# Optimization experiments

Measured on AMD Instinct MI355X. Metric: run time of the kernel, lower is better.

## Reference

```python
import jax, jax.numpy as jnp
import numpy as np

HIDDEN = 128
NUM_BLOCKS = 8
BLOCK = HIDDEN // NUM_BLOCKS  # 16
HSF = 1                       # hidden_size_factor
LAMBDA = 0.01                 # sparsity_threshold (softshrink)
SCALE = 0.02


def softshrink(v, lam):
    return jnp.sign(v) * jnp.maximum(jnp.abs(v) - lam, 0.0)


def setup_inputs() -> dict:
    key = jax.random.key(0)
    k0, k1, k2, k3, k4 = jax.random.split(key, 5)
    x = jax.random.normal(k0, (4, HIDDEN, 256, 256), dtype=jnp.float32)
    w1 = SCALE * jax.random.normal(k1, (2, NUM_BLOCKS, BLOCK, BLOCK * HSF), dtype=jnp.float32)
    b1 = SCALE * jax.random.normal(k2, (2, NUM_BLOCKS, BLOCK * HSF), dtype=jnp.float32)
    w2 = SCALE * jax.random.normal(k3, (2, NUM_BLOCKS, BLOCK * HSF, BLOCK), dtype=jnp.float32)
    b2 = SCALE * jax.random.normal(k4, (2, NUM_BLOCKS, BLOCK), dtype=jnp.float32)
    return {"x": x, "w1": w1, "b1": b1, "w2": w2, "b2": b2}


def reference(x, w1, b1, w2, b2):
    bias = x
    B, C, H, W = x.shape
    xf = jnp.fft.rfft2(x.astype(jnp.float32), axes=(2, 3), norm='ortho')  # [B,C,H,Wf] complex
    Wf = xf.shape[3]
    xb = xf.reshape(B, NUM_BLOCKS, BLOCK, H, Wf)
    xr, xi = xb.real, xb.imag

    mm = lambda a, w: jnp.einsum('bkihw,kio->bkohw', a, w)
    o1r = jax.nn.relu(mm(xr, w1[0]) - mm(xi, w1[1]) + b1[0][None, :, :, None, None])
    o1i = jax.nn.relu(mm(xi, w1[0]) + mm(xr, w1[1]) + b1[1][None, :, :, None, None])
    o2r = mm(o1r, w2[0]) - mm(o1i, w2[1]) + b2[0][None, :, :, None, None]
    o2i = mm(o1i, w2[0]) + mm(o1r, w2[1]) + b2[1][None, :, :, None, None]

    sr = softshrink(o2r, LAMBDA)
    si = softshrink(o2i, LAMBDA)
    xc = (sr + 1j * si).reshape(B, C, H, Wf) * xf
    out = jnp.fft.irfft2(xc, s=(H, W), axes=(2, 3), norm='ortho').astype(x.dtype)
    return out + bias
```

## Files before the change

### kernel.cpp

```cpp
#include <hip/hip_runtime.h>
#include <math.h>

#define Bn 4
#define Cn 128
#define Hn 256
#define Wn 256
#define WFn 129
#define NBn 8
#define BLn 16
#define LAMv 0.01f
#define LSTR 272

#define C1c 0.9238795325112867f
#define S1c 0.3826834323650898f
#define RTc 0.7071067811865476f

__device__ constexpr int rev4(int j) {
  return ((j & 1) << 3) | ((j & 2) << 1) | ((j & 4) >> 1) | ((j & 8) >> 3);
}

__device__ __forceinline__ float2 pkfma(float2 a, float2 b, float2 c) {
  return make_float2(fmaf(a.x, b.x, c.x), fmaf(a.y, b.y, c.y));
}

__device__ __forceinline__ void init_twt(float2* twt, int t) {
  int s = t >> 4, k2 = t & 15;
  float sn, cs;
  sincospif((float)(s * k2) / 128.0f, &sn, &cs);
  twt[t] = make_float2(cs, -sn);
}

template <int SIGN>
__device__ __forceinline__ void fft16(float* xr, float* xi) {
  const float g = (SIGN > 0) ? 1.0f : -1.0f;
  {
    const float WC[8] = {1.f, C1c, RTc, S1c, 0.f, -S1c, -RTc, -C1c};
    const float WS[8] = {0.f, -S1c, -RTc, -C1c, -1.f, -C1c, -RTc, -S1c};
#pragma unroll
    for (int j = 0; j < 8; j++) {
      float ur = xr[j], ui = xi[j], vr = xr[j + 8], vi = xi[j + 8];
      float dr = ur - vr, di = ui - vi;
      xr[j] = ur + vr; xi[j] = ui + vi;
      float wc = WC[j], ws = g * WS[j];
      xr[j + 8] = dr * wc - di * ws;
      xi[j + 8] = dr * ws + di * wc;
    }
  }
  {
    const float WC[4] = {1.f, RTc, 0.f, -RTc};
    const float WS[4] = {0.f, -RTc, -1.f, -RTc};
#pragma unroll
    for (int b = 0; b < 16; b += 8)
#pragma unroll
      for (int j = 0; j < 4; j++) {
        float ur = xr[b + j], ui = xi[b + j];
        float vr = xr[b + j + 4], vi = xi[b + j + 4];
        float dr = ur - vr, di = ui - vi;
        xr[b + j] = ur + vr; xi[b + j] = ui + vi;
        float wc = WC[j], ws = g * WS[j];
        xr[b + j + 4] = dr * wc - di * ws;
        xi[b + j + 4] = dr * ws + di * wc;
      }
  }
  {
#pragma unroll
    for (int b = 0; b < 16; b += 4) {
      {
        float ur = xr[b], ui = xi[b], vr = xr[b + 2], vi = xi[b + 2];
        xr[b] = ur + vr; xi[b] = ui + vi;
        xr[b + 2] = ur - vr; xi[b + 2] = ui - vi;
      }
      {
        float ur = xr[b + 1], ui = xi[b + 1], vr = xr[b + 3], vi = xi[b + 3];
        float dr = ur - vr, di = ui - vi;
        xr[b + 1] = ur + vr; xi[b + 1] = ui + vi;
        xr[b + 3] = g * di;
        xi[b + 3] = -g * dr;
      }
    }
  }
  {
#pragma unroll
    for (int b = 0; b < 16; b += 2) {
      float ur = xr[b], ui = xi[b], vr = xr[b + 1], vi = xi[b + 1];
      xr[b] = ur + vr; xi[b] = ui + vi;
      xr[b + 1] = ur - vr; xi[b + 1] = ui - vi;
    }
  }
}

template <int SIGN>
__device__ __forceinline__ void fft256_4step(float* vr, float* vi,
                                             float* re, float* im, int s,
                                             const float2* twt) {
  fft16<SIGN>(vr, vi);
#pragma unroll
  for (int j = 1; j < 16; j++) {
    const int k2 = rev4(j);
    float2 w = twt[s * 16 + k2];
    float wc = w.x;
    float ws = (SIGN > 0) ? w.y : -w.y;
    float r = vr[j] * wc - vi[j] * ws;
    vi[j] = vr[j] * ws + vi[j] * wc;
    vr[j] = r;
  }
  __syncthreads();
#pragma unroll
  for (int j = 0; j < 16; j++) {
    const int k2 = rev4(j);
    const int p = k2 * 16 + (s ^ k2);
    re[p] = vr[j]; im[p] = vi[j];
  }
  __syncthreads();
#pragma unroll
  for (int n1 = 0; n1 < 16; n1++) {
    const int p = s * 16 + (n1 ^ s);
    vr[n1] = re[p]; vi[n1] = im[p];
  }
  __syncthreads();
  fft16<SIGN>(vr, vi);
}

__global__ __launch_bounds__(256) void k_rowfft(const float* __restrict__ x,
                                                float2* __restrict__ S) {
  int blk = blockIdx.x;
  int bc = blk >> 3;
  int h0 = (blk & 7) << 5;
  __shared__ __align__(16) float zr[16][LSTR], zi[16][LSTR];
  __shared__ __align__(16) float2 twt[256];
  int t = threadIdx.x;
  init_twt(&twt[0], t);
  const float4* xrow =
      (const float4*)(x + (size_t)bc * (Hn * Wn) + (size_t)h0 * Wn);
  const float sc = 1.0f / 256.0f;
#pragma unroll
  for (int j = 0; j < 8; j++) {
    int f4 = t + j * 256;
    float4 v = xrow[f4];
    int r = f4 >> 6;
    int i = (f4 << 2) & 255;
    float* dst = (r & 1) ? &zi[r >> 1][i] : &zr[r >> 1][i];
    *(float4*)dst = make_float4(v.x * sc, v.y * sc, v.z * sc, v.w * sc);
  }
  __syncthreads();
  int p = t >> 4, s = t & 15;
  float vr[16], vi[16];
#pragma unroll
  for (int m = 0; m < 16; m++) {
    vr[m] = zr[p][s + 16 * m];
    vi[m] = zi[p][s + 16 * m];
  }
  fft256_4step<1>(vr, vi, &zr[p][0], &zi[p][0], s, &twt[0]);
#pragma unroll
  for (int j = 0; j < 16; j++) {
    int h = 16 * rev4(j) + s;
    zr[p][h] = vr[j]; zi[p][h] = vi[j];
  }
  __syncthreads();
  for (int f = t; f < WFn * 32; f += 256) {
    int wf = f >> 5, rr = f & 31;
    int pp = rr >> 1;
    int nk = (256 - wf) & 255;
    float zkr = zr[pp][wf], zki = zi[pp][wf];
    float znr = zr[pp][nk], zni = zi[pp][nk];
    float re_, im_;
    if ((rr & 1) == 0) { re_ = 0.5f * (zkr + znr); im_ = 0.5f * (zki - zni); }
    else               { re_ = 0.5f * (zki + zni); im_ = 0.5f * (znr - zkr); }
    S[((size_t)bc * WFn + wf) * Hn + (h0 + rr)] = make_float2(re_, im_);
  }
}

__global__ __launch_bounds__(256) void k_spectral(float2* __restrict__ S,
                                                  const float* __restrict__ w1,
                                                  const float* __restrict__ b1,
                                                  const float* __restrict__ w2,
                                                  const float* __restrict__ b2) {
  int blk = blockIdx.x;
  int wcol = blk % WFn;
  int bk = blk / WFn;
  int k = bk & 7;
  int b = bk >> 3;
  __shared__ __align__(16) float ar[16][LSTR], ai[16][LSTR];
  __shared__ __align__(16) float2 twt[256];
  __shared__ __align__(16) float w1r[256], w1i[256], w2r[256], w2i[256];
  __shared__ float b1r[16], b1i[16], b2r[16], b2i[16];
  int t = threadIdx.x;
  init_twt(&twt[0], t);
  w1r[t] = w1[k * 256 + t];        w1i[t] = w1[(8 + k) * 256 + t];
  w2r[t] = w2[k * 256 + t];        w2i[t] = w2[(8 + k) * 256 + t];
  if (t < 16) {
    b1r[t] = b1[k * 16 + t];       b1i[t] = b1[(8 + k) * 16 + t];
    b2r[t] = b2[k * 16 + t];       b2i[t] = b2[(8 + k) * 16 + t];
  }
  __syncthreads();
  int c = t >> 4, s = t & 15;
  float2* col = S + ((size_t)(b * Cn + k * BLn + c) * WFn + wcol) * Hn;
  float vr[16], vi[16];
#pragma unroll
  for (int m = 0; m < 16; m++) {
    float2 z = col[s + 16 * m];
    vr[m] = z.x; vi[m] = z.y;
  }
  fft256_4step<1>(vr, vi, &ar[c][0], &ai[c][0], s, &twt[0]);
#pragma unroll
  for (int j = 0; j < 16; j++) {
    int h = 16 * rev4(j) + s;
    ar[c][h] = vr[j]; ai[c][h] = vi[j];
  }
  __syncthreads();

  {
    const int h = t;
    const float4* W1R = (const float4*)w1r;
    const float4* W1I = (const float4*)w1i;
    const float4* W2R = (const float4*)w2r;
    const float4* W2I = (const float4*)w2i;
    float2 o1p[8], o1q[8];
#pragma unroll
    for (int q = 0; q < 8; q++) {
      o1p[q] = make_float2(b1r[2 * q], b1r[2 * q + 1]);
      o1q[q] = make_float2(b1i[2 * q], b1i[2 * q + 1]);
    }
#pragma unroll
    for (int i = 0; i < 16; i++) {
      float xr_ = ar[i][h], xi_ = ai[i][h];
      float2 xr2 = make_float2(xr_, xr_);
      float2 xi2 = make_float2(xi_, xi_);
      float2 xn2 = make_float2(-xi_, -xi_);
#pragma unroll
      for (int oq = 0; oq < 4; oq++) {
        float4 wr = W1R[i * 4 + oq];
        float4 wi = W1I[i * 4 + oq];
        float2 wr0 = make_float2(wr.x, wr.y), wr1 = make_float2(wr.z, wr.w);
        float2 wi0 = make_float2(wi.x, wi.y), wi1 = make_float2(wi.z, wi.w);
        o1p[2 * oq + 0] = pkfma(xr2, wr0, pkfma(xn2, wi0, o1p[2 * oq + 0]));
        o1p[2 * oq + 1] = pkfma(xr2, wr1, pkfma(xn2, wi1, o1p[2 * oq + 1]));
        o1q[2 * oq + 0] = pkfma(xi2, wr0, pkfma(xr2, wi0, o1q[2 * oq + 0]));
        o1q[2 * oq + 1] = pkfma(xi2, wr1, pkfma(xr2, wi1, o1q[2 * oq + 1]));
      }
    }
#pragma unroll
    for (int q = 0; q < 8; q++) {
      o1p[q] = make_float2(fmaxf(o1p[q].x, 0.f), fmaxf(o1p[q].y, 0.f));
      o1q[q] = make_float2(fmaxf(o1q[q].x, 0.f), fmaxf(o1q[q].y, 0.f));
    }
    float2 o2p[8], o2q[8];
#pragma unroll
    for (int q = 0; q < 8; q++) {
      o2p[q] = make_float2(b2r[2 * q], b2r[2 * q + 1]);
      o2q[q] = make_float2(b2i[2 * q], b2i[2 * q + 1]);
    }
#pragma unroll
    for (int i = 0; i < 16; i++) {
      float pr = (i & 1) ? o1p[i >> 1].y : o1p[i >> 1].x;
      float pi_ = (i & 1) ? o1q[i >> 1].y : o1q[i >> 1].x;
      float2 pr2 = make_float2(pr, pr);
      float2 pi2 = make_float2(pi_, pi_);
      float2 pn2 = make_float2(-pi_, -pi_);
#pragma unroll
      for (int oq = 0; oq < 4; oq++) {
        float4 wr = W2R[i * 4 + oq];
        float4 wi = W2I[i * 4 + oq];
        float2 wr0 = make_float2(wr.x, wr.y), wr1 = make_float2(wr.z, wr.w);
        float2 wi0 = make_float2(wi.x, wi.y), wi1 = make_float2(wi.z, wi.w);
        o2p[2 * oq + 0] = pkfma(pr2, wr0, pkfma(pn2, wi0, o2p[2 * oq + 0]));
        o2p[2 * oq + 1] = pkfma(pr2, wr1, pkfma(pn2, wi1, o2p[2 * oq + 1]));
        o2q[2 * oq + 0] = pkfma(pi2, wr0, pkfma(pr2, wi0, o2q[2 * oq + 0]));
        o2q[2 * oq + 1] = pkfma(pi2, wr1, pkfma(pr2, wi1, o2q[2 * oq + 1]));
      }
    }
#pragma unroll
    for (int o = 0; o < 16; o++) {
      float vr_ = (o & 1) ? o2p[o >> 1].y : o2p[o >> 1].x;
      float vi_ = (o & 1) ? o2q[o >> 1].y : o2q[o >> 1].x;
      float sr = copysignf(fmaxf(fabsf(vr_) - LAMv, 0.0f), vr_);
      float si = copysignf(fmaxf(fabsf(vi_) - LAMv, 0.0f), vi_);
      float fr = ar[o][h], fi = ai[o][h];
      ar[o][h] = sr * fr - si * fi;
      ai[o][h] = sr * fi + si * fr;
    }
  }
  __syncthreads();
#pragma unroll
  for (int m = 0; m < 16; m++) {
    vr[m] = ar[c][s + 16 * m];
    vi[m] = ai[c][s + 16 * m];
  }
  fft256_4step<-1>(vr, vi, &ar[c][0], &ai[c][0], s, &twt[0]);
#pragma unroll
  for (int j = 0; j < 16; j++) {
    int h = 16 * rev4(j) + s;
    col[h] = make_float2(vr[j], vi[j]);
  }
}

__global__ __launch_bounds__(256) void k_invrow(const float2* __restrict__ S,
                                                const float* __restrict__ x,
                                                float* __restrict__ out) {
  int blk = blockIdx.x;
  int bc = blk >> 3;
  int h0 = (blk & 7) << 5;
  __shared__ __align__(16) float zr[16][LSTR], zi[16][LSTR];
  __shared__ __align__(16) float2 twt[256];
  int t = threadIdx.x;
  init_twt(&twt[0], t);
  const float4* S4 = (const float4*)S;
  for (int f = t; f < WFn * 16; f += 256) {
    int wf = f >> 4, p = f & 15;
    float4 v = S4[((size_t)bc * WFn + wf) * (Hn / 2) + (h0 >> 1) + p];
    zr[p][wf] = v.x - v.w;
    zi[p][wf] = v.y + v.z;
    if (wf >= 1 && wf <= 127) {
      zr[p][256 - wf] = v.x + v.w;
      zi[p][256 - wf] = v.z - v.y;
    }
  }
  __syncthreads();
  int p = t >> 4, s = t & 15;
  float vr[16], vi[16];
#pragma unroll
  for (int m = 0; m < 16; m++) {
    vr[m] = zr[p][s + 16 * m];
    vi[m] = zi[p][s + 16 * m];
  }
  fft256_4step<-1>(vr, vi, &zr[p][0], &zi[p][0], s, &twt[0]);
#pragma unroll
  for (int j = 0; j < 16; j++) {
    int w = 16 * rev4(j) + s;
    zr[p][w] = vr[j]; zi[p][w] = vi[j];
  }
  __syncthreads();
  const float sc = 1.0f / 256.0f;
  size_t base = (size_t)bc * (Hn * Wn) + (size_t)h0 * Wn;
  const float4* x4 = (const float4*)(x + base);
  float4* o4 = (float4*)(out + base);
#pragma unroll
  for (int j = 0; j < 8; j++) {
    int f4 = t + j * 256;
    int rr = f4 >> 6;
    int i = (f4 << 2) & 255;
    const float* src = (rr & 1) ? &zi[rr >> 1][i] : &zr[rr >> 1][i];
    float4 v = *(const float4*)src;
    float4 xv = x4[f4];
    o4[f4] = make_float4(fmaf(v.x, sc, xv.x), fmaf(v.y, sc, xv.y),
                         fmaf(v.z, sc, xv.z), fmaf(v.w, sc, xv.w));
  }
}

extern "C" void kernel_launch(void* const* d_in, const int* in_sizes, int n_in,
                              void* d_out, int out_size, void* d_ws,
                              size_t ws_size, hipStream_t stream) {
  const float* x  = (const float*)d_in[0];
  const float* w1 = (const float*)d_in[1];
  const float* b1 = (const float*)d_in[2];
  const float* w2 = (const float*)d_in[3];
  const float* b2 = (const float*)d_in[4];
  float* out = (float*)d_out;
  float2* S = (float2*)d_ws;

  k_rowfft<<<Bn * Cn * (Hn / 32), 256, 0, stream>>>(x, S);
  k_spectral<<<Bn * NBn * WFn, 256, 0, stream>>>(S, w1, b1, w2, b2);
  k_invrow<<<Bn * Cn * (Hn / 32), 256, 0, stream>>>(S, x, out);
}
```

Measured before the change: 458.5 us.

## Process two frequency columns per block in spectral kernel

Each spectral block now handles two adjacent Wf columns, so the twiddle table, weight and bias loads into shared memory are paid once per two columns. The grid shrinks to 65 column pairs per (b,k), and the MLP loop interleaves two independent accumulator sets to give more ILP. The twiddle table is also transposed so that lanes with consecutive s read consecutive entries, which should cut LDS bank conflicts. In exchange, shared memory per block roughly doubles and register pressure rises, which may lower occupancy, and the odd last column runs redundant FFT work on leftover data.

```diff
diff --git a/kernel.cpp b/kernel.cpp
--- a/kernel.cpp
+++ b/kernel.cpp
@@ -24,7 +24,7 @@
 }
 
 __device__ __forceinline__ void init_twt(float2* twt, int t) {
-  int s = t >> 4, k2 = t & 15;
+  int k2 = t >> 4, s = t & 15;
   float sn, cs;
   sincospif((float)(s * k2) / 128.0f, &sn, &cs);
   twt[t] = make_float2(cs, -sn);
@@ -97,7 +97,7 @@
 #pragma unroll
   for (int j = 1; j < 16; j++) {
     const int k2 = rev4(j);
-    float2 w = twt[s * 16 + k2];
+    float2 w = twt[k2 * 16 + s];
     float wc = w.x;
     float ws = (SIGN > 0) ? w.y : -w.y;
     float r = vr[j] * wc - vi[j] * ws;
@@ -176,11 +176,13 @@
                                                   const float* __restrict__ w2,
                                                   const float* __restrict__ b2) {
   int blk = blockIdx.x;
-  int wcol = blk % WFn;
-  int bk = blk / WFn;
+  int wi = blk % 65;
+  int bk = blk / 65;
   int k = bk & 7;
   int b = bk >> 3;
-  __shared__ __align__(16) float ar[16][LSTR], ai[16][LSTR];
+  int wcol0 = wi * 2;
+  const bool has1 = (wcol0 + 1) < WFn;
+  __shared__ __align__(16) float ar[2][16][LSTR], ai[2][16][LSTR];
   __shared__ __align__(16) float2 twt[256];
   __shared__ __align__(16) float w1r[256], w1i[256], w2r[256], w2i[256];
   __shared__ float b1r[16], b1i[16], b2r[16], b2i[16];
@@ -194,18 +196,32 @@
   }
   __syncthreads();
   int c = t >> 4, s = t & 15;
-  float2* col = S + ((size_t)(b * Cn + k * BLn + c) * WFn + wcol) * Hn;
+  float2* col0 = S + ((size_t)(b * Cn + k * BLn + c) * WFn + wcol0) * Hn;
+  float2* col1 = col0 + Hn;
   float vr[16], vi[16];
 #pragma unroll
   for (int m = 0; m < 16; m++) {
-    float2 z = col[s + 16 * m];
+    float2 z = col0[s + 16 * m];
     vr[m] = z.x; vi[m] = z.y;
   }
-  fft256_4step<1>(vr, vi, &ar[c][0], &ai[c][0], s, &twt[0]);
+  fft256_4step<1>(vr, vi, &ar[0][c][0], &ai[0][c][0], s, &twt[0]);
 #pragma unroll
   for (int j = 0; j < 16; j++) {
     int h = 16 * rev4(j) + s;
-    ar[c][h] = vr[j]; ai[c][h] = vi[j];
+    ar[0][c][h] = vr[j]; ai[0][c][h] = vi[j];
+  }
+  if (has1) {
+#pragma unroll
+    for (int m = 0; m < 16; m++) {
+      float2 z = col1[s + 16 * m];
+      vr[m] = z.x; vi[m] = z.y;
+    }
+  }
+  fft256_4step<1>(vr, vi, &ar[1][c][0], &ai[1][c][0], s, &twt[0]);
+#pragma unroll
+  for (int j = 0; j < 16; j++) {
+    int h = 16 * rev4(j) + s;
+    ar[1][c][h] = vr[j]; ai[1][c][h] = vi[j];
   }
   __syncthreads();
 
@@ -215,82 +231,116 @@
     const float4* W1I = (const float4*)w1i;
     const float4* W2R = (const float4*)w2r;
     const float4* W2I = (const float4*)w2i;
-    float2 o1p[8], o1q[8];
+    float2 o1p[2][8], o1q[2][8];
 #pragma unroll
     for (int q = 0; q < 8; q++) {
-      o1p[q] = make_float2(b1r[2 * q], b1r[2 * q + 1]);
-      o1q[q] = make_float2(b1i[2 * q], b1i[2 * q + 1]);
+      float2 bp = make_float2(b1r[2 * q], b1r[2 * q + 1]);
+      float2 bq = make_float2(b1i[2 * q], b1i[2 * q + 1]);
+      o1p[0][q] = bp; o1p[1][q] = bp;
+      o1q[0][q] = bq; o1q[1][q] = bq;
     }
 #pragma unroll
     for (int i = 0; i < 16; i++) {
-      float xr_ = ar[i][h], xi_ = ai[i][h];
-      float2 xr2 = make_float2(xr_, xr_);
-      float2 xi2 = make_float2(xi_, xi_);
-      float2 xn2 = make_float2(-xi_, -xi_);
+      float xr0 = ar[0][i][h], xi0 = ai[0][i][h];
+      float xr1 = ar[1][i][h], xi1 = ai[1][i][h];
+      float2 xr20 = make_float2(xr0, xr0), xi20 = make_float2(xi0, xi0);
+      float2 xn20 = make_float2(-xi0, -xi0);
+      float2 xr21 = make_float2(xr1, xr1), xi21 = make_float2(xi1, xi1);
+      float2 xn21 = make_float2(-xi1, -xi1);
 #pragma unroll
       for (int oq = 0; oq < 4; oq++) {
         float4 wr = W1R[i * 4 + oq];
         float4 wi = W1I[i * 4 + oq];
         float2 wr0 = make_float2(wr.x, wr.y), wr1 = make_float2(wr.z, wr.w);
         float2 wi0 = make_float2(wi.x, wi.y), wi1 = make_float2(wi.z, wi.w);
-        o1p[2 * oq + 0] = pkfma(xr2, wr0, pkfma(xn2, wi0, o1p[2 * oq + 0]));
-        o1p[2 * oq + 1] = pkfma(xr2, wr1, pkfma(xn2, wi1, o1p[2 * oq + 1]));
-        o1q[2 * oq + 0] = pkfma(xi2, wr0, pkfma(xr2, wi0, o1q[2 * oq + 0]));
-        o1q[2 * oq + 1] = pkfma(xi2, wr1, pkfma(xr2, wi1, o1q[2 * oq + 1]));
-      }
-    }
+        o1p[0][2*oq+0] = pkfma(xr20, wr0, pkfma(xn20, wi0, o1p[0][2*oq+0]));
+        o1p[0][2*oq+1] = pkfma(xr20, wr1, pkfma(xn20, wi1, o1p[0][2*oq+1]));
+        o1q[0][2*oq+0] = pkfma(xi20, wr0, pkfma(xr20, wi0, o1q[0][2*oq+0]));
+        o1q[0][2*oq+1] = pkfma(xi20, wr1, pkfma(xr20, wi1, o1q[0][2*oq+1]));
+        o1p[1][2*oq+0] = pkfma(xr21, wr0, pkfma(xn21, wi0, o1p[1][2*oq+0]));
+        o1p[1][2*oq+1] = pkfma(xr21, wr1, pkfma(xn21, wi1, o1p[1][2*oq+1]));
+        o1q[1][2*oq+0] = pkfma(xi21, wr0, pkfma(xr21, wi0, o1q[1][2*oq+0]));
+        o1q[1][2*oq+1] = pkfma(xi21, wr1, pkfma(xr21, wi1, o1q[1][2*oq+1]));
+      }
+    }
+#pragma unroll
+    for (int u = 0; u < 2; u++)
+#pragma unroll
+      for (int q = 0; q < 8; q++) {
+        o1p[u][q] = make_float2(fmaxf(o1p[u][q].x, 0.f), fmaxf(o1p[u][q].y, 0.f));
+        o1q[u][q] = make_float2(fmaxf(o1q[u][q].x, 0.f), fmaxf(o1q[u][q].y, 0.f));
+      }
+    float2 o2p[2][8], o2q[2][8];
 #pragma unroll
     for (int q = 0; q < 8; q++) {
-      o1p[q] = make_float2(fmaxf(o1p[q].x, 0.f), fmaxf(o1p[q].y, 0.f));
-      o1q[q] = make_float2(fmaxf(o1q[q].x, 0.f), fmaxf(o1q[q].y, 0.f));
-    }
-    float2 o2p[8], o2q[8];
-#pragma unroll
-    for (int q = 0; q < 8; q++) {
-      o2p[q] = make_float2(b2r[2 * q], b2r[2 * q + 1]);
-      o2q[q] = make_float2(b2i[2 * q], b2i[2 * q + 1]);
+      float2 bp = make_float2(b2r[2 * q], b2r[2 * q + 1]);
+      float2 bq = make_float2(b2i[2 * q], b2i[2 * q + 1]);
+      o2p[0][q] = bp; o2p[1][q] = bp;
+      o2q[0][q] = bq; o2q[1][q] = bq;
     }
 #pragma unroll
     for (int i = 0; i < 16; i++) {
-      float pr = (i & 1) ? o1p[i >> 1].y : o1p[i >> 1].x;
-      float pi_ = (i & 1) ? o1q[i >> 1].y : o1q[i >> 1].x;
-      float2 pr2 = make_float2(pr, pr);
-      float2 pi2 = make_float2(pi_, pi_);
-      float2 pn2 = make_float2(-pi_, -pi_);
+      float pr0 = (i & 1) ? o1p[0][i >> 1].y : o1p[0][i >> 1].x;
+      float pi0 = (i & 1) ? o1q[0][i >> 1].y : o1q[0][i >> 1].x;
+      float pr1 = (i & 1) ? o1p[1][i >> 1].y : o1p[1][i >> 1].x;
+      float pi1 = (i & 1) ? o1q[1][i >> 1].y : o1q[1][i >> 1].x;
+      float2 pr20 = make_float2(pr0, pr0), pi20 = make_float2(pi0, pi0);
+      float2 pn20 = make_float2(-pi0, -pi0);
+      float2 pr21 = make_float2(pr1, pr1), pi21 = make_float2(pi1, pi1);
+      float2 pn21 = make_float2(-pi1, -pi1);
 #pragma unroll
       for (int oq = 0; oq < 4; oq++) {
         float4 wr = W2R[i * 4 + oq];
         float4 wi = W2I[i * 4 + oq];
         float2 wr0 = make_float2(wr.x, wr.y), wr1 = make_float2(wr.z, wr.w);
         float2 wi0 = make_float2(wi.x, wi.y), wi1 = make_float2(wi.z, wi.w);
-        o2p[2 * oq + 0] = pkfma(pr2, wr0, pkfma(pn2, wi0, o2p[2 * oq + 0]));
-        o2p[2 * oq + 1] = pkfma(pr2, wr1, pkfma(pn2, wi1, o2p[2 * oq + 1]));
-        o2q[2 * oq + 0] = pkfma(pi2, wr0, pkfma(pr2, wi0, o2q[2 * oq + 0]));
-        o2q[2 * oq + 1] = pkfma(pi2, wr1, pkfma(pr2, wi1, o2q[2 * oq + 1]));
-      }
-    }
-#pragma unroll
-    for (int o = 0; o < 16; o++) {
-      float vr_ = (o & 1) ? o2p[o >> 1].y : o2p[o >> 1].x;
-      float vi_ = (o & 1) ? o2q[o >> 1].y : o2q[o >> 1].x;
-      float sr = copysignf(fmaxf(fabsf(vr_) - LAMv, 0.0f), vr_);
-      float si = copysignf(fmaxf(fabsf(vi_) - LAMv, 0.0f), vi_);
-      float fr = ar[o][h], fi = ai[o][h];
-      ar[o][h] = sr * fr - si * fi;
-      ai[o][h] = sr * fi + si * fr;
-    }
+        o2p[0][2*oq+0] = pkfma(pr20, wr0, pkfma(pn20, wi0, o2p[0][2*oq+0]));
+        o2p[0][2*oq+1] = pkfma(pr20, wr1, pkfma(pn20, wi1, o2p[0][2*oq+1]));
+        o2q[0][2*oq+0] = pkfma(pi20, wr0, pkfma(pr20, wi0, o2q[0][2*oq+0]));
+        o2q[0][2*oq+1] = pkfma(pi20, wr1, pkfma(pr20, wi1, o2q[0][2*oq+1]));
+        o2p[1][2*oq+0] = pkfma(pr21, wr0, pkfma(pn21, wi0, o2p[1][2*oq+0]));
+        o2p[1][2*oq+1] = pkfma(pr21, wr1, pkfma(pn21, wi1, o2p[1][2*oq+1]));
+        o2q[1][2*oq+0] = pkfma(pi21, wr0, pkfma(pr21, wi0, o2q[1][2*oq+0]));
+        o2q[1][2*oq+1] = pkfma(pi21, wr1, pkfma(pr21, wi1, o2q[1][2*oq+1]));
+      }
+    }
+#pragma unroll
+    for (int u = 0; u < 2; u++)
+#pragma unroll
+      for (int o = 0; o < 16; o++) {
+        float vr_ = (o & 1) ? o2p[u][o >> 1].y : o2p[u][o >> 1].x;
+        float vi_ = (o & 1) ? o2q[u][o >> 1].y : o2q[u][o >> 1].x;
+        float sr = copysignf(fmaxf(fabsf(vr_) - LAMv, 0.0f), vr_);
+        float si = copysignf(fmaxf(fabsf(vi_) - LAMv, 0.0f), vi_);
+        float fr = ar[u][o][h], fi = ai[u][o][h];
+        ar[u][o][h] = sr * fr - si * fi;
+        ai[u][o][h] = sr * fi + si * fr;
+      }
   }
   __syncthreads();
 #pragma unroll
   for (int m = 0; m < 16; m++) {
-    vr[m] = ar[c][s + 16 * m];
-    vi[m] = ai[c][s + 16 * m];
-  }
-  fft256_4step<-1>(vr, vi, &ar[c][0], &ai[c][0], s, &twt[0]);
+    vr[m] = ar[0][c][s + 16 * m];
+    vi[m] = ai[0][c][s + 16 * m];
+  }
+  fft256_4step<-1>(vr, vi, &ar[0][c][0], &ai[0][c][0], s, &twt[0]);
 #pragma unroll
   for (int j = 0; j < 16; j++) {
     int h = 16 * rev4(j) + s;
-    col[h] = make_float2(vr[j], vi[j]);
+    col0[h] = make_float2(vr[j], vi[j]);
+  }
+#pragma unroll
+  for (int m = 0; m < 16; m++) {
+    vr[m] = ar[1][c][s + 16 * m];
+    vi[m] = ai[1][c][s + 16 * m];
+  }
+  fft256_4step<-1>(vr, vi, &ar[1][c][0], &ai[1][c][0], s, &twt[0]);
+  if (has1) {
+#pragma unroll
+    for (int j = 0; j < 16; j++) {
+      int h = 16 * rev4(j) + s;
+      col1[h] = make_float2(vr[j], vi[j]);
+    }
   }
 }
 
@@ -359,6 +409,6 @@
   float2* S = (float2*)d_ws;
 
   k_rowfft<<<Bn * Cn * (Hn / 32), 256, 0, stream>>>(x, S);
-  k_spectral<<<Bn * NBn * WFn, 256, 0, stream>>>(S, w1, b1, w2, b2);
+  k_spectral<<<Bn * NBn * 65, 256, 0, stream>>>(S, w1, b1, w2, b2);
   k_invrow<<<Bn * Cn * (Hn / 32), 256, 0, stream>>>(S, x, out);
 }
```

New measurement: 421.7 us. -8.0%, faster.
